# Optimization experiments

Measured on AMD Instinct MI355X. Metric: run time of the kernel, lower is better.

The kernel has to match this reference:

```python
import jax, jax.numpy as jnp
import numpy as np

N, S, T, D = 8, 2048, 2048, 1024


def setup_inputs() -> dict:
    key0 = jax.random.key(0)
    ks = jax.random.split(key0, 6)
    scale = 1.0 / np.sqrt(D).astype(np.float32)
    query = jax.random.normal(ks[0], (N, S, D), dtype=jnp.float32)
    key = jax.random.normal(ks[1], (N, T, D), dtype=jnp.float32)
    value = jax.random.normal(ks[2], (N, T, D), dtype=jnp.float32)
    # nn.Linear(D, D, bias=False) weights, shape [out, in]
    Wq = jax.random.normal(ks[3], (D, D), dtype=jnp.float32) * scale
    Wk = jax.random.normal(ks[4], (D, D), dtype=jnp.float32) * scale
    Wv = jax.random.normal(ks[5], (D, D), dtype=jnp.float32) * scale
    # causal mask: 1 on/below diagonal, 0 above (zeros become -inf additively)
    attn_mask = jnp.tril(jnp.ones((S, T), dtype=jnp.float32))
    return {"key": key, "query": query, "value": value,
            "Wq": Wq, "Wk": Wk, "Wv": Wv, "attn_mask": attn_mask}


def reference(key, query, value, Wq, Wk, Wv, attn_mask):
    d = query.shape[-1]
    q = query @ Wq.T              # [N,S,D]
    k = key @ Wk.T                # [N,T,D]
    v = value @ Wv.T              # [N,T,D]
    scores = jnp.einsum('nsd,ntd->nst', q, k)          # [N,S,T]
    # masked_fill(mask==0, -inf) then ADD the (nonzero) mask values
    additive = jnp.where(attn_mask == 0, -jnp.inf, attn_mask)
    scores = scores + additive                          # broadcast [S,T] -> [N,S,T]
    # NOTE: torch code divides by D**(-0.5), i.e. multiplies by sqrt(D). Faithful.
    attn = jax.nn.softmax(scores * jnp.sqrt(jnp.float32(d)), axis=-1)
    return jnp.einsum('nst,ntd->nsd', attn, v)          # [N,S,D]
```

## Files before the change

kernel.cpp:

```cpp
#include <hip/hip_runtime.h>
#include <hip/hip_bf16.h>


typedef __attribute__((ext_vector_type(4))) float f32x4;
typedef __attribute__((ext_vector_type(8))) short bf16x8;
typedef __attribute__((ext_vector_type(4))) short s16x4;

#define DEVI __device__ __forceinline__

DEVI unsigned short f2bf(float x) {
  union { float f; unsigned u; } v; v.f = x;
  unsigned r = v.u + 0x7FFFu + ((v.u >> 16) & 1u);
  return (unsigned short)(r >> 16);
}
DEVI float bf2f(unsigned short b) {
  union { float f; unsigned u; } v; v.u = ((unsigned)b) << 16;
  return v.f;
}

DEVI void gload16(const void* g, void* l) {
#if __has_builtin(__builtin_amdgcn_global_load_lds)
  typedef __attribute__((address_space(1))) const unsigned int* gas_u32;
  typedef __attribute__((address_space(3))) unsigned int* las_u32;
  __builtin_amdgcn_global_load_lds(
      (gas_u32)(unsigned long long)g,
      (las_u32)(unsigned int)(unsigned long long)l, 16, 0, 0);
#else
  *(bf16x8*)l = *(const bf16x8*)g;
#endif
}

DEVI int xcd_swizzle(int bid, int nwg) {
  if (nwg & 7) return bid;
  int cpx = nwg >> 3;
  return (bid & 7) * cpx + (bid >> 3);
}

constexpr int NB = 8, SS = 2048, TT = 2048, DD = 1024;
constexpr long long TILE_E = 16384;

__global__ __launch_bounds__(256) void split_hl_k(
    const float* __restrict__ in, unsigned short* __restrict__ hi,
    unsigned short* __restrict__ lo, long long n4)
{
  long long i = (long long)blockIdx.x * 256 + threadIdx.x;
  long long stride = (long long)gridDim.x * 256;
  for (; i < n4; i += stride) {
    f32x4 v = ((const f32x4*)in)[i];
    s16x4 h, l;
#pragma unroll
    for (int e = 0; e < 4; ++e) {
      unsigned short hh = f2bf(v[e]);
      h[e] = (short)hh;
      l[e] = (short)f2bf(v[e] - bf2f(hh));
    }
    ((s16x4*)hi)[i] = h;
    ((s16x4*)lo)[i] = l;
  }
}

__global__ __launch_bounds__(256) void split_h_k(
    const float* __restrict__ in, unsigned short* __restrict__ hi, long long n4)
{
  long long i = (long long)blockIdx.x * 256 + threadIdx.x;
  long long stride = (long long)gridDim.x * 256;
  for (; i < n4; i += stride) {
    f32x4 v = ((const f32x4*)in)[i];
    s16x4 h;
#pragma unroll
    for (int e = 0; e < 4; ++e) h[e] = (short)f2bf(v[e]);
    ((s16x4*)hi)[i] = h;
  }
}

template<int NMFMA, bool SPLIT_OUT>
__global__ __launch_bounds__(256, 2) void gemm_bt(
    const unsigned short* __restrict__ Ah_g, const unsigned short* __restrict__ Al_g,
    const unsigned short* __restrict__ Bh_g, const unsigned short* __restrict__ Bl_g,
    unsigned short* __restrict__ Chi, unsigned short* __restrict__ Clo,
    int Nn, int K,
    long long aStride, long long bStride, long long cStride,
    int tilesM, int tilesN)
{
  __shared__ short lds[(NMFMA == 3 ? 4 : 2) * 8192];
  short* Ah = lds;
  short* Al = (NMFMA == 3) ? lds + 8192 : nullptr;
  short* Bh = lds + (NMFMA == 3 ? 16384 : 8192);
  short* Bl = (NMFMA == 3) ? lds + 24576 : nullptr;

  int tid = threadIdx.x;
  int lane = tid & 63, wid = tid >> 6;
  int wr = wid >> 1, wc = wid & 1;
  int l15 = lane & 15, lq = lane >> 4;

  int wg = xcd_swizzle(blockIdx.x, gridDim.x);
  int tilesPer = tilesM * tilesN;
  int b = wg / tilesPer;
  int rem = wg % tilesPer;
  int mt = rem / tilesN, nt = rem % tilesN;

  const unsigned short* Agh = Ah_g + (long long)b * aStride + (long long)mt * 128 * K;
  const unsigned short* Bgh = Bh_g + (long long)b * bStride + (long long)nt * 128 * K;
  const unsigned short* Agl = nullptr; const unsigned short* Bgl = nullptr;
  if constexpr (NMFMA == 3) {
    Agl = Al_g + (long long)b * aStride + (long long)mt * 128 * K;
    Bgl = Bl_g + (long long)b * bStride + (long long)nt * 128 * K;
  }

  f32x4 acc[4][4];
#pragma unroll
  for (int i = 0; i < 4; ++i)
#pragma unroll
    for (int j = 0; j < 4; ++j) acc[i][j] = (f32x4){0.f, 0.f, 0.f, 0.f};

  for (int k0 = 0; k0 < K; k0 += 64) {
    __syncthreads();
#pragma unroll
    for (int it = 0; it < 4; ++it) {
      int ii = it * 256 + tid;
      int r = ii >> 3;
      int c8 = (ii & 7) ^ (r & 7);
      long long go = (long long)r * K + k0 + c8 * 8;
      gload16(Agh + go, &Ah[ii * 8]);
      gload16(Bgh + go, &Bh[ii * 8]);
      if constexpr (NMFMA == 3) {
        gload16(Agl + go, &Al[ii * 8]);
        gload16(Bgl + go, &Bl[ii * 8]);
      }
    }
    __syncthreads();
#pragma unroll
    for (int kk = 0; kk < 64; kk += 32) {
      bf16x8 afh[4], afl[4], bfh[4], bfl[4];
#pragma unroll
      for (int i = 0; i < 4; ++i) {
        int row = wr * 64 + i * 16 + l15;
        int bo = (row * 128 + (kk + lq * 8) * 2) ^ ((row & 7) << 4);
        afh[i] = *(const bf16x8*)(&Ah[bo >> 1]);
        if constexpr (NMFMA == 3) afl[i] = *(const bf16x8*)(&Al[bo >> 1]);
        int col = wc * 64 + i * 16 + l15;
        int bo2 = (col * 128 + (kk + lq * 8) * 2) ^ ((col & 7) << 4);
        bfh[i] = *(const bf16x8*)(&Bh[bo2 >> 1]);
        if constexpr (NMFMA == 3) bfl[i] = *(const bf16x8*)(&Bl[bo2 >> 1]);
      }
#pragma unroll
      for (int i = 0; i < 4; ++i)
#pragma unroll
        for (int j = 0; j < 4; ++j) {
          acc[i][j] = __builtin_amdgcn_mfma_f32_16x16x32_bf16(afh[i], bfh[j], acc[i][j], 0, 0, 0);
          if constexpr (NMFMA == 3) {
            acc[i][j] = __builtin_amdgcn_mfma_f32_16x16x32_bf16(afh[i], bfl[j], acc[i][j], 0, 0, 0);
            acc[i][j] = __builtin_amdgcn_mfma_f32_16x16x32_bf16(afl[i], bfh[j], acc[i][j], 0, 0, 0);
          }
        }
    }
  }

  unsigned short* ch = Chi + (long long)b * cStride;
  unsigned short* cl = SPLIT_OUT ? (Clo + (long long)b * cStride) : nullptr;
#pragma unroll
  for (int i = 0; i < 4; ++i)
#pragma unroll
    for (int j = 0; j < 4; ++j)
#pragma unroll
      for (int e = 0; e < 4; ++e) {
        int row = mt * 128 + wr * 64 + i * 16 + lq * 4 + e;
        int col = nt * 128 + wc * 64 + j * 16 + l15;
        float vv = acc[i][j][e];
        unsigned short h = f2bf(vv);
        ch[(long long)row * Nn + col] = h;
        if constexpr (SPLIT_OUT) cl[(long long)row * Nn + col] = f2bf(vv - bf2f(h));
      }
}

__global__ __launch_bounds__(256, 2) void qk_bt(
    const unsigned short* __restrict__ qh, const unsigned short* __restrict__ ql,
    const unsigned short* __restrict__ kh, const unsigned short* __restrict__ kl,
    float* __restrict__ Sg)
{
  __shared__ short lds[4 * 8192];
  short* Ah = lds;
  short* Al = lds + 8192;
  short* Bh = lds + 16384;
  short* Bl = lds + 24576;

  int tid = threadIdx.x;
  int lane = tid & 63, wid = tid >> 6;
  int wr = wid >> 1, wc = wid & 1;
  int l15 = lane & 15, lq = lane >> 4;

  int wg = xcd_swizzle(blockIdx.x, gridDim.x);
  int b = wg / 136;
  int idx = wg % 136;
  int st = (int)((sqrtf(8.f * (float)idx + 1.f) - 1.f) * 0.5f);
  while ((st + 1) * (st + 2) / 2 <= idx) ++st;
  while (st * (st + 1) / 2 > idx) --st;
  int tt = idx - st * (st + 1) / 2;

  const unsigned short* Agh = qh + (long long)b * SS * DD + (long long)st * 128 * DD;
  const unsigned short* Agl = ql + (long long)b * SS * DD + (long long)st * 128 * DD;
  const unsigned short* Bgh = kh + (long long)b * TT * DD + (long long)tt * 128 * DD;
  const unsigned short* Bgl = kl + (long long)b * TT * DD + (long long)tt * 128 * DD;

  f32x4 acc[4][4];
#pragma unroll
  for (int i = 0; i < 4; ++i)
#pragma unroll
    for (int j = 0; j < 4; ++j) acc[i][j] = (f32x4){0.f, 0.f, 0.f, 0.f};

  for (int k0 = 0; k0 < DD; k0 += 64) {
    __syncthreads();
#pragma unroll
    for (int it = 0; it < 4; ++it) {
      int ii = it * 256 + tid;
      int r = ii >> 3;
      int c8 = (ii & 7) ^ (r & 7);
      long long go = (long long)r * DD + k0 + c8 * 8;
      gload16(Agh + go, &Ah[ii * 8]);
      gload16(Agl + go, &Al[ii * 8]);
      gload16(Bgh + go, &Bh[ii * 8]);
      gload16(Bgl + go, &Bl[ii * 8]);
    }
    __syncthreads();
#pragma unroll
    for (int kk = 0; kk < 64; kk += 32) {
      bf16x8 afh[4], afl[4], bfh[4], bfl[4];
#pragma unroll
      for (int i = 0; i < 4; ++i) {
        int row = wr * 64 + i * 16 + l15;
        int bo = (row * 128 + (kk + lq * 8) * 2) ^ ((row & 7) << 4);
        afh[i] = *(const bf16x8*)(&Ah[bo >> 1]);
        afl[i] = *(const bf16x8*)(&Al[bo >> 1]);
        int col = wc * 64 + i * 16 + l15;
        int bo2 = (col * 128 + (kk + lq * 8) * 2) ^ ((col & 7) << 4);
        bfh[i] = *(const bf16x8*)(&Bh[bo2 >> 1]);
        bfl[i] = *(const bf16x8*)(&Bl[bo2 >> 1]);
      }
#pragma unroll
      for (int i = 0; i < 4; ++i)
#pragma unroll
        for (int j = 0; j < 4; ++j) {
          acc[i][j] = __builtin_amdgcn_mfma_f32_16x16x32_bf16(afh[i], bfh[j], acc[i][j], 0, 0, 0);
          acc[i][j] = __builtin_amdgcn_mfma_f32_16x16x32_bf16(afh[i], bfl[j], acc[i][j], 0, 0, 0);
          acc[i][j] = __builtin_amdgcn_mfma_f32_16x16x32_bf16(afl[i], bfh[j], acc[i][j], 0, 0, 0);
        }
    }
  }

  float* Sb = Sg + ((long long)b * 136 + idx) * TILE_E;
#pragma unroll
  for (int i = 0; i < 4; ++i)
#pragma unroll
    for (int j = 0; j < 4; ++j)
#pragma unroll
      for (int e = 0; e < 4; ++e) {
        int row = wr * 64 + i * 16 + lq * 4 + e;
        int col = wc * 64 + j * 16 + l15;
        Sb[(long long)row * 128 + col] = acc[i][j][e];
      }
}

__global__ __launch_bounds__(256) void softmax_kernel(float* __restrict__ Sg)
{
  __shared__ float red[8];
  int blk = blockIdx.x;
  int b = blk >> 11, s = blk & 2047;
  int st = s >> 7, r = s & 127;
  long long tri = (long long)st * (st + 1) / 2;
  const float* tb = Sg + ((long long)b * 136 + tri) * TILE_E + (long long)r * 128;

  int tid = threadIdx.x;
  int lane = tid & 63, wid = tid >> 6;

  int c0 = tid * 8;
  int tt = c0 >> 7, cc = c0 & 127;
  bool live = (c0 <= s);
  f32x4 v0 = {0.f, 0.f, 0.f, 0.f}, v1 = {0.f, 0.f, 0.f, 0.f};
  if (live) {
    const float* seg = tb + (long long)tt * TILE_E + cc;
    v0 = *(const f32x4*)seg;
    v1 = *(const f32x4*)(seg + 4);
  }

  float m = -3.0e38f;
#pragma unroll
  for (int e = 0; e < 4; ++e) {
    if (c0 + e <= s) m = fmaxf(m, v0[e]);
    if (c0 + 4 + e <= s) m = fmaxf(m, v1[e]);
  }
#pragma unroll
  for (int o = 32; o > 0; o >>= 1) m = fmaxf(m, __shfl_xor(m, o));
  if (lane == 0) red[wid] = m;
  __syncthreads();
  m = fmaxf(fmaxf(red[0], red[1]), fmaxf(red[2], red[3]));

  const float C = 46.16624130844683f;
  float p0[4], p1[4];
  float sum = 0.f;
#pragma unroll
  for (int e = 0; e < 4; ++e) {
    p0[e] = (c0 + e <= s) ? exp2f((v0[e] - m) * C) : 0.f;
    sum += p0[e];
    p1[e] = (c0 + 4 + e <= s) ? exp2f((v1[e] - m) * C) : 0.f;
    sum += p1[e];
  }
#pragma unroll
  for (int o = 32; o > 0; o >>= 1) sum += __shfl_xor(sum, o);
  if (lane == 0) red[4 + wid] = sum;
  __syncthreads();
  float inv = 1.f / (red[4] + red[5] + red[6] + red[7]);

  union { bf16x8 v; s16x4 h[2]; } w;
#pragma unroll
  for (int e = 0; e < 4; ++e) {
    w.h[0][e] = (short)f2bf(p0[e] * inv);
    w.h[1][e] = (short)f2bf(p1[e] * inv);
  }
  __syncthreads();
  if (c0 < (st + 1) * 128) {
    unsigned short* pw = (unsigned short*)Sg +
        (((long long)b * 136 + tri + tt) * TILE_E) * 2 + (long long)r * 256 + cc;
    *(bf16x8*)pw = w.v;
  }
}

__global__ __launch_bounds__(256, 2) void pv_bt(
    const unsigned short* __restrict__ P, const unsigned short* __restrict__ vT,
    float* __restrict__ Out)
{
  __shared__ short lds[2 * 8192];
  short* Ah = lds;
  short* Bh = lds + 8192;

  int tid = threadIdx.x;
  int lane = tid & 63, wid = tid >> 6;
  int wr = wid >> 1, wc = wid & 1;
  int l15 = lane & 15, lq = lane >> 4;

  int wg = xcd_swizzle(blockIdx.x, gridDim.x);
  int b = wg >> 7;
  int rem = wg & 127;
  int st = rem >> 3, dt = rem & 7;

  const unsigned short* Ps = P + ((long long)b * 136 + (long long)st * (st + 1) / 2) * (TILE_E * 2);
  const unsigned short* Vb = vT + (long long)b * DD * TT + (long long)dt * 128 * TT;
  int nkt = (st + 1) * 2;

  f32x4 acc[4][4];
#pragma unroll
  for (int i = 0; i < 4; ++i)
#pragma unroll
    for (int j = 0; j < 4; ++j) acc[i][j] = (f32x4){0.f, 0.f, 0.f, 0.f};

  for (int kt = 0; kt < nkt; ++kt) {
    int ttk = kt >> 1, ck = (kt & 1) * 64;
    __syncthreads();
#pragma unroll
    for (int it = 0; it < 4; ++it) {
      int ii = it * 256 + tid;
      int r = ii >> 3;
      int c8 = (ii & 7) ^ (r & 7);
      gload16(Ps + (long long)ttk * (TILE_E * 2) + (long long)r * 256 + ck + c8 * 8, &Ah[ii * 8]);
      gload16(Vb + (long long)r * TT + kt * 64 + c8 * 8, &Bh[ii * 8]);
    }
    __syncthreads();
#pragma unroll
    for (int kk = 0; kk < 64; kk += 32) {
      bf16x8 af[4], bfr[4];
#pragma unroll
      for (int i = 0; i < 4; ++i) {
        int row = wr * 64 + i * 16 + l15;
        int bo = (row * 128 + (kk + lq * 8) * 2) ^ ((row & 7) << 4);
        af[i] = *(const bf16x8*)(&Ah[bo >> 1]);
        int col = wc * 64 + i * 16 + l15;
        int bo2 = (col * 128 + (kk + lq * 8) * 2) ^ ((col & 7) << 4);
        bfr[i] = *(const bf16x8*)(&Bh[bo2 >> 1]);
      }
#pragma unroll
      for (int i = 0; i < 4; ++i)
#pragma unroll
        for (int j = 0; j < 4; ++j)
          acc[i][j] = __builtin_amdgcn_mfma_f32_16x16x32_bf16(af[i], bfr[j], acc[i][j], 0, 0, 0);
    }
  }

  float* Ob = Out + (long long)b * SS * DD;
#pragma unroll
  for (int i = 0; i < 4; ++i)
#pragma unroll
    for (int j = 0; j < 4; ++j)
#pragma unroll
      for (int e = 0; e < 4; ++e) {
        int row = st * 128 + wr * 64 + i * 16 + lq * 4 + e;
        int col = dt * 128 + wc * 64 + j * 16 + l15;
        Ob[(long long)row * DD + col] = acc[i][j][e];
      }
}

extern "C" void kernel_launch(void* const* d_in, const int* in_sizes, int n_in,
                              void* d_out, int out_size, void* d_ws, size_t ws_size,
                              hipStream_t stream) {
  (void)in_sizes; (void)n_in; (void)out_size;
  const float* key   = (const float*)d_in[0];
  const float* query = (const float*)d_in[1];
  const float* value = (const float*)d_in[2];
  const float* Wq    = (const float*)d_in[3];
  const float* Wk    = (const float*)d_in[4];
  const float* Wv    = (const float*)d_in[5];
  float* Out = (float*)d_out;

  const long long SD = (long long)SS * DD;
  const long long DT = (long long)DD * TT;
  const long long WN = (long long)DD * DD;

  const unsigned long long PLANE_B  = (unsigned long long)SD * 2;
  const unsigned long long WPLANE_B = (unsigned long long)WN * 2;
  const unsigned long long SCORE_B  = 136ull * TILE_E * 4;

  auto need = [&](int g) -> unsigned long long {
    return 5ull * WPLANE_B + (unsigned long long)g * (SCORE_B + 5ull * PLANE_B);
  };
  int G = 1;
  for (int g : {8, 4, 2, 1}) if (ws_size >= need(g)) { G = g; break; }

  char* ws = (char*)d_ws;
  size_t off = 0;
  auto alloc = [&](unsigned long long bytes) { char* p = ws + off; off += bytes; return p; };

  unsigned short* wqh = (unsigned short*)alloc(WPLANE_B);
  unsigned short* wql = (unsigned short*)alloc(WPLANE_B);
  unsigned short* wkh = (unsigned short*)alloc(WPLANE_B);
  unsigned short* wkl = (unsigned short*)alloc(WPLANE_B);
  unsigned short* wvh = (unsigned short*)alloc(WPLANE_B);
  char* slab = alloc((unsigned long long)G * SCORE_B);
  unsigned short* qh  = (unsigned short*)alloc((unsigned long long)G * PLANE_B);
  unsigned short* ql  = (unsigned short*)alloc((unsigned long long)G * PLANE_B);
  unsigned short* kh  = (unsigned short*)alloc((unsigned long long)G * PLANE_B);
  unsigned short* kl  = (unsigned short*)alloc((unsigned long long)G * PLANE_B);
  unsigned short* vT  = (unsigned short*)alloc((unsigned long long)G * PLANE_B);

  unsigned short* iah = (unsigned short*)slab;
  unsigned short* ial = (unsigned short*)(slab + (unsigned long long)G * PLANE_B);
  float* Sg = (float*)slab;

  split_hl_k<<<512, 256, 0, stream>>>(Wq, wqh, wql, WN / 4);
  split_hl_k<<<512, 256, 0, stream>>>(Wk, wkh, wkl, WN / 4);
  split_h_k<<<512, 256, 0, stream>>>(Wv, wvh, WN / 4);

  for (int b0 = 0; b0 < NB; b0 += G) {
    long long n4 = (long long)G * SD / 4;
    split_hl_k<<<2048, 256, 0, stream>>>(query + (long long)b0 * SD, iah, ial, n4);
    gemm_bt<3, true><<<G * 128, 256, 0, stream>>>(
        iah, ial, wqh, wql, qh, ql, DD, DD, SD, 0, SD, 16, 8);
    split_hl_k<<<2048, 256, 0, stream>>>(key + (long long)b0 * SD, iah, ial, n4);
    gemm_bt<3, true><<<G * 128, 256, 0, stream>>>(
        iah, ial, wkh, wkl, kh, kl, DD, DD, SD, 0, SD, 16, 8);
    split_h_k<<<2048, 256, 0, stream>>>(value + (long long)b0 * SD, iah, n4);
    gemm_bt<1, false><<<G * 128, 256, 0, stream>>>(
        wvh, nullptr, iah, nullptr, vT, nullptr, TT, DD, 0, SD, DT, 8, 16);
    qk_bt<<<G * 136, 256, 0, stream>>>(qh, ql, kh, kl, Sg);
    softmax_kernel<<<G * SS, 256, 0, stream>>>(Sg);
    pv_bt<<<G * 128, 256, 0, stream>>>(
        (const unsigned short*)Sg, vT, Out + (long long)b0 * SD);
  }
}
```

Baseline: 526.8 us.

## Double-buffer LDS staging with K=32 halves to overlap global loads and MFMA

Restructures the three GEMM kernels (projection, QK, PV) so each LDS region is split into two K=32 halves that are staged alternately. The next half's global-to-LDS loads are issued before computing on the current half, and the two paired operands (hi/lo or A/B) are packed side by side in each 128-byte row. The goal is to overlap memory latency with MFMA work instead of serialising load, sync and compute. In exchange, each step now does only one k-slice between barriers, so there are more __syncthreads per unit of work.

Result: no change. 530.0 us (+0.6%).

```diff
diff --git a/kernel.cpp b/kernel.cpp
--- a/kernel.cpp
+++ b/kernel.cpp
@@ -36,6 +36,21 @@
   return (bid & 7) * cpx + (bid >> 3);
 }
 
+DEVI void stage_pair(const unsigned short* __restrict__ s0, long long rs0,
+                     const unsigned short* __restrict__ s1, long long rs1,
+                     short* lds, int tid) {
+#pragma unroll
+  for (int it = 0; it < 4; ++it) {
+    int ii = it * 256 + tid;
+    int r = ii >> 3;
+    int c8 = (ii & 7) ^ (r & 7);
+    const unsigned short* src = (c8 < 4)
+        ? s0 + (long long)r * rs0 + (c8 & 3) * 8
+        : s1 + (long long)r * rs1 + (c8 & 3) * 8;
+    gload16(src, &lds[ii * 8]);
+  }
+}
+
 constexpr int NB = 8, SS = 2048, TT = 2048, DD = 1024;
 constexpr long long TILE_E = 16384;
 
@@ -82,11 +97,8 @@
     long long aStride, long long bStride, long long cStride,
     int tilesM, int tilesN)
 {
-  __shared__ short lds[(NMFMA == 3 ? 4 : 2) * 8192];
-  short* Ah = lds;
-  short* Al = (NMFMA == 3) ? lds + 8192 : nullptr;
-  short* Bh = lds + (NMFMA == 3 ? 16384 : 8192);
-  short* Bl = (NMFMA == 3) ? lds + 24576 : nullptr;
+  constexpr int NBUF = (NMFMA == 3) ? 4 : 2;
+  __shared__ short lds[NBUF * 8192];
 
   int tid = threadIdx.x;
   int lane = tid & 63, wid = tid >> 6;
@@ -101,11 +113,8 @@
 
   const unsigned short* Agh = Ah_g + (long long)b * aStride + (long long)mt * 128 * K;
   const unsigned short* Bgh = Bh_g + (long long)b * bStride + (long long)nt * 128 * K;
-  const unsigned short* Agl = nullptr; const unsigned short* Bgl = nullptr;
-  if constexpr (NMFMA == 3) {
-    Agl = Al_g + (long long)b * aStride + (long long)mt * 128 * K;
-    Bgl = Bl_g + (long long)b * bStride + (long long)nt * 128 * K;
-  }
+  const unsigned short* Agl = (NMFMA == 3) ? Al_g + (long long)b * aStride + (long long)mt * 128 * K : nullptr;
+  const unsigned short* Bgl = (NMFMA == 3) ? Bl_g + (long long)b * bStride + (long long)nt * 128 * K : nullptr;
 
   f32x4 acc[4][4];
 #pragma unroll
@@ -113,47 +122,68 @@
 #pragma unroll
     for (int j = 0; j < 4; ++j) acc[i][j] = (f32x4){0.f, 0.f, 0.f, 0.f};
 
-  for (int k0 = 0; k0 < K; k0 += 64) {
-    __syncthreads();
-#pragma unroll
-    for (int it = 0; it < 4; ++it) {
-      int ii = it * 256 + tid;
-      int r = ii >> 3;
-      int c8 = (ii & 7) ^ (r & 7);
-      long long go = (long long)r * K + k0 + c8 * 8;
-      gload16(Agh + go, &Ah[ii * 8]);
-      gload16(Bgh + go, &Bh[ii * 8]);
-      if constexpr (NMFMA == 3) {
-        gload16(Agl + go, &Al[ii * 8]);
-        gload16(Bgl + go, &Bl[ii * 8]);
-      }
+  auto stage = [&](int t, int half) {
+    int k0 = t * 32;
+    if constexpr (NMFMA == 3) {
+      stage_pair(Agh + k0, K, Agl + k0, K, lds + half * 16384, tid);
+      stage_pair(Bgh + k0, K, Bgl + k0, K, lds + half * 16384 + 8192, tid);
+    } else {
+      stage_pair(Agh + k0, K, Bgh + k0, K, lds + half * 8192, tid);
     }
-    __syncthreads();
-#pragma unroll
-    for (int kk = 0; kk < 64; kk += 32) {
+  };
+
+  auto compute = [&](int half) {
+    if constexpr (NMFMA == 3) {
+      const short* U = lds + half * 16384;
+      const short* Vb2 = U + 8192;
       bf16x8 afh[4], afl[4], bfh[4], bfl[4];
 #pragma unroll
       for (int i = 0; i < 4; ++i) {
-        int row = wr * 64 + i * 16 + l15;
-        int bo = (row * 128 + (kk + lq * 8) * 2) ^ ((row & 7) << 4);
-        afh[i] = *(const bf16x8*)(&Ah[bo >> 1]);
-        if constexpr (NMFMA == 3) afl[i] = *(const bf16x8*)(&Al[bo >> 1]);
-        int col = wc * 64 + i * 16 + l15;
-        int bo2 = (col * 128 + (kk + lq * 8) * 2) ^ ((col & 7) << 4);
-        bfh[i] = *(const bf16x8*)(&Bh[bo2 >> 1]);
-        if constexpr (NMFMA == 3) bfl[i] = *(const bf16x8*)(&Bl[bo2 >> 1]);
+        int ra = wr * 64 + i * 16 + l15;
+        int sa = (ra & 7) << 4;
+        afh[i] = *(const bf16x8*)(&U[((ra * 128 + lq * 16) ^ sa) >> 1]);
+        afl[i] = *(const bf16x8*)(&U[((ra * 128 + 64 + lq * 16) ^ sa) >> 1]);
+        int rb = wc * 64 + i * 16 + l15;
+        int sb = (rb & 7) << 4;
+        bfh[i] = *(const bf16x8*)(&Vb2[((rb * 128 + lq * 16) ^ sb) >> 1]);
+        bfl[i] = *(const bf16x8*)(&Vb2[((rb * 128 + 64 + lq * 16) ^ sb) >> 1]);
       }
 #pragma unroll
       for (int i = 0; i < 4; ++i)
 #pragma unroll
         for (int j = 0; j < 4; ++j) {
           acc[i][j] = __builtin_amdgcn_mfma_f32_16x16x32_bf16(afh[i], bfh[j], acc[i][j], 0, 0, 0);
-          if constexpr (NMFMA == 3) {
-            acc[i][j] = __builtin_amdgcn_mfma_f32_16x16x32_bf16(afh[i], bfl[j], acc[i][j], 0, 0, 0);
-            acc[i][j] = __builtin_amdgcn_mfma_f32_16x16x32_bf16(afl[i], bfh[j], acc[i][j], 0, 0, 0);
-          }
+          acc[i][j] = __builtin_amdgcn_mfma_f32_16x16x32_bf16(afh[i], bfl[j], acc[i][j], 0, 0, 0);
+          acc[i][j] = __builtin_amdgcn_mfma_f32_16x16x32_bf16(afl[i], bfh[j], acc[i][j], 0, 0, 0);
         }
+    } else {
+      const short* W = lds + half * 8192;
+      bf16x8 af[4], bfr[4];
+#pragma unroll
+      for (int i = 0; i < 4; ++i) {
+        int ra = wr * 64 + i * 16 + l15;
+        af[i] = *(const bf16x8*)(&W[((ra * 128 + lq * 16) ^ ((ra & 7) << 4)) >> 1]);
+        int rb = wc * 64 + i * 16 + l15;
+        bfr[i] = *(const bf16x8*)(&W[((rb * 128 + 64 + lq * 16) ^ ((rb & 7) << 4)) >> 1]);
+      }
+#pragma unroll
+      for (int i = 0; i < 4; ++i)
+#pragma unroll
+        for (int j = 0; j < 4; ++j)
+          acc[i][j] = __builtin_amdgcn_mfma_f32_16x16x32_bf16(af[i], bfr[j], acc[i][j], 0, 0, 0);
     }
+  };
+
+  int NT = K >> 5;
+  stage(0, 0);
+  __syncthreads();
+  for (int t = 0; t < NT; t += 2) {
+    if (t + 1 < NT) stage(t + 1, 1);
+    compute(0);
+    __syncthreads();
+    if (t + 2 < NT) stage(t + 2, 0);
+    compute(1);
+    __syncthreads();
   }
 
   unsigned short* ch = Chi + (long long)b * cStride;
@@ -179,10 +209,6 @@
     float* __restrict__ Sg)
 {
   __shared__ short lds[4 * 8192];
-  short* Ah = lds;
-  short* Al = lds + 8192;
-  short* Bh = lds + 16384;
-  short* Bl = lds + 24576;
 
   int tid = threadIdx.x;
   int lane = tid & 63, wid = tid >> 6;
@@ -208,43 +234,45 @@
 #pragma unroll
     for (int j = 0; j < 4; ++j) acc[i][j] = (f32x4){0.f, 0.f, 0.f, 0.f};
 
-  for (int k0 = 0; k0 < DD; k0 += 64) {
-    __syncthreads();
-#pragma unroll
-    for (int it = 0; it < 4; ++it) {
-      int ii = it * 256 + tid;
-      int r = ii >> 3;
-      int c8 = (ii & 7) ^ (r & 7);
-      long long go = (long long)r * DD + k0 + c8 * 8;
-      gload16(Agh + go, &Ah[ii * 8]);
-      gload16(Agl + go, &Al[ii * 8]);
-      gload16(Bgh + go, &Bh[ii * 8]);
-      gload16(Bgl + go, &Bl[ii * 8]);
+  auto stage = [&](int t, int half) {
+    int k0 = t * 32;
+    stage_pair(Agh + k0, DD, Agl + k0, DD, lds + half * 16384, tid);
+    stage_pair(Bgh + k0, DD, Bgl + k0, DD, lds + half * 16384 + 8192, tid);
+  };
+  auto compute = [&](int half) {
+    const short* U = lds + half * 16384;
+    const short* Vb2 = U + 8192;
+    bf16x8 afh[4], afl[4], bfh[4], bfl[4];
+#pragma unroll
+    for (int i = 0; i < 4; ++i) {
+      int ra = wr * 64 + i * 16 + l15;
+      int sa = (ra & 7) << 4;
+      afh[i] = *(const bf16x8*)(&U[((ra * 128 + lq * 16) ^ sa) >> 1]);
+      afl[i] = *(const bf16x8*)(&U[((ra * 128 + 64 + lq * 16) ^ sa) >> 1]);
+      int rb = wc * 64 + i * 16 + l15;
+      int sb = (rb & 7) << 4;
+      bfh[i] = *(const bf16x8*)(&Vb2[((rb * 128 + lq * 16) ^ sb) >> 1]);
+      bfl[i] = *(const bf16x8*)(&Vb2[((rb * 128 + 64 + lq * 16) ^ sb) >> 1]);
     }
-    __syncthreads();
-#pragma unroll
-    for (int kk = 0; kk < 64; kk += 32) {
-      bf16x8 afh[4], afl[4], bfh[4], bfl[4];
-#pragma unroll
-      for (int i = 0; i < 4; ++i) {
-        int row = wr * 64 + i * 16 + l15;
-        int bo = (row * 128 + (kk + lq * 8) * 2) ^ ((row & 7) << 4);
-        afh[i] = *(const bf16x8*)(&Ah[bo >> 1]);
-        afl[i] = *(const bf16x8*)(&Al[bo >> 1]);
-        int col = wc * 64 + i * 16 + l15;
-        int bo2 = (col * 128 + (kk + lq * 8) * 2) ^ ((col & 7) << 4);
-        bfh[i] = *(const bf16x8*)(&Bh[bo2 >> 1]);
-        bfl[i] = *(const bf16x8*)(&Bl[bo2 >> 1]);
-      }
-#pragma unroll
-      for (int i = 0; i < 4; ++i)
-#pragma unroll
-        for (int j = 0; j < 4; ++j) {
-          acc[i][j] = __builtin_amdgcn_mfma_f32_16x16x32_bf16(afh[i], bfh[j], acc[i][j], 0, 0, 0);
-          acc[i][j] = __builtin_amdgcn_mfma_f32_16x16x32_bf16(afh[i], bfl[j], acc[i][j], 0, 0, 0);
-          acc[i][j] = __builtin_amdgcn_mfma_f32_16x16x32_bf16(afl[i], bfh[j], acc[i][j], 0, 0, 0);
-        }
-    }
+#pragma unroll
+    for (int i = 0; i < 4; ++i)
+#pragma unroll
+      for (int j = 0; j < 4; ++j) {
+        acc[i][j] = __builtin_amdgcn_mfma_f32_16x16x32_bf16(afh[i], bfh[j], acc[i][j], 0, 0, 0);
+        acc[i][j] = __builtin_amdgcn_mfma_f32_16x16x32_bf16(afh[i], bfl[j], acc[i][j], 0, 0, 0);
+        acc[i][j] = __builtin_amdgcn_mfma_f32_16x16x32_bf16(afl[i], bfh[j], acc[i][j], 0, 0, 0);
+      }
+  };
+
+  stage(0, 0);
+  __syncthreads();
+  for (int t = 0; t < 32; t += 2) {
+    if (t + 1 < 32) stage(t + 1, 1);
+    compute(0);
+    __syncthreads();
+    if (t + 2 < 32) stage(t + 2, 0);
+    compute(1);
+    __syncthreads();
   }
 
   float* Sb = Sg + ((long long)b * 136 + idx) * TILE_E;
@@ -329,8 +357,6 @@
     float* __restrict__ Out)
 {
   __shared__ short lds[2 * 8192];
-  short* Ah = lds;
-  short* Bh = lds + 8192;
 
   int tid = threadIdx.x;
   int lane = tid & 63, wid = tid >> 6;
@@ -344,7 +370,7 @@
 
   const unsigned short* Ps = P + ((long long)b * 136 + (long long)st * (st + 1) / 2) * (TILE_E * 2);
   const unsigned short* Vb = vT + (long long)b * DD * TT + (long long)dt * 128 * TT;
-  int nkt = (st + 1) * 2;
+  int NT = (st + 1) * 4;
 
   f32x4 acc[4][4];
 #pragma unroll
@@ -352,36 +378,37 @@
 #pragma unroll
     for (int j = 0; j < 4; ++j) acc[i][j] = (f32x4){0.f, 0.f, 0.f, 0.f};
 
-  for (int kt = 0; kt < nkt; ++kt) {
-    int ttk = kt >> 1, ck = (kt & 1) * 64;
-    __syncthreads();
-#pragma unroll
-    for (int it = 0; it < 4; ++it) {
-      int ii = it * 256 + tid;
-      int r = ii >> 3;
-      int c8 = (ii & 7) ^ (r & 7);
-      gload16(Ps + (long long)ttk * (TILE_E * 2) + (long long)r * 256 + ck + c8 * 8, &Ah[ii * 8]);
-      gload16(Vb + (long long)r * TT + kt * 64 + c8 * 8, &Bh[ii * 8]);
+  auto stage = [&](int t, int half) {
+    int t0 = t * 32;
+    const unsigned short* s0 = Ps + (long long)(t0 >> 7) * (TILE_E * 2) + (t0 & 127);
+    stage_pair(s0, 256, Vb + t0, TT, lds + half * 8192, tid);
+  };
+  auto compute = [&](int half) {
+    const short* W = lds + half * 8192;
+    bf16x8 af[4], bfr[4];
+#pragma unroll
+    for (int i = 0; i < 4; ++i) {
+      int ra = wr * 64 + i * 16 + l15;
+      af[i] = *(const bf16x8*)(&W[((ra * 128 + lq * 16) ^ ((ra & 7) << 4)) >> 1]);
+      int rb = wc * 64 + i * 16 + l15;
+      bfr[i] = *(const bf16x8*)(&W[((rb * 128 + 64 + lq * 16) ^ ((rb & 7) << 4)) >> 1]);
     }
-    __syncthreads();
-#pragma unroll
-    for (int kk = 0; kk < 64; kk += 32) {
-      bf16x8 af[4], bfr[4];
-#pragma unroll
-      for (int i = 0; i < 4; ++i) {
-        int row = wr * 64 + i * 16 + l15;
-        int bo = (row * 128 + (kk + lq * 8) * 2) ^ ((row & 7) << 4);
-        af[i] = *(const bf16x8*)(&Ah[bo >> 1]);
-        int col = wc * 64 + i * 16 + l15;
-        int bo2 = (col * 128 + (kk + lq * 8) * 2) ^ ((col & 7) << 4);
-        bfr[i] = *(const bf16x8*)(&Bh[bo2 >> 1]);
-      }
-#pragma unroll
-      for (int i = 0; i < 4; ++i)
-#pragma unroll
-        for (int j = 0; j < 4; ++j)
-          acc[i][j] = __builtin_amdgcn_mfma_f32_16x16x32_bf16(af[i], bfr[j], acc[i][j], 0, 0, 0);
-    }
+#pragma unroll
+    for (int i = 0; i < 4; ++i)
+#pragma unroll
+      for (int j = 0; j < 4; ++j)
+        acc[i][j] = __builtin_amdgcn_mfma_f32_16x16x32_bf16(af[i], bfr[j], acc[i][j], 0, 0, 0);
+  };
+
+  stage(0, 0);
+  __syncthreads();
+  for (int t = 0; t < NT; t += 2) {
+    if (t + 1 < NT) stage(t + 1, 1);
+    compute(0);
+    __syncthreads();
+    if (t + 2 < NT) stage(t + 2, 0);
+    compute(1);
+    __syncthreads();
   }
 
   float* Ob = Out + (long long)b * SS * DD;
```
